# Optimization experiments

Hardware: AMD Instinct MI355X
Metric: run time of the kernel (lower is better)

Reference implementation:

```python
import jax, jax.numpy as jnp
import numpy as np

T = 0.2          # temperature
W = 0.1          # loss weight
BIG = 2 ** 30    # sentinel label for masked-out samples


def setup_inputs() -> dict:
    key = jax.random.key(0)
    k1, k2, k3, k4 = jax.random.split(key, 4)
    bs, C, Gn, S = 32, 128, 256, 16
    grouped_features = jax.random.normal(k1, (bs, C, Gn, S), dtype=jnp.float32)
    # instance labels in [-1, 8): -1 = background
    proposal_instance_mask = jax.random.randint(k2, (bs, Gn, S), -1, 8, dtype=jnp.int32)
    # seed indices with duplicates possible (range 40 over 16 samples)
    grouped_indices = jax.random.randint(k3, (bs, Gn, S), 0, 40, dtype=jnp.int32)
    context_compen = jax.random.normal(k4, (1, C), dtype=jnp.float32)
    return {
        "proposal_instance_mask": proposal_instance_mask,
        "grouped_features": grouped_features,
        "grouped_indices": grouped_indices,
        "context_compen": context_compen,
    }


def _group_loss(feat, idx, lab, ctx):
    # feat: [S, C], idx: [S], lab: [S], ctx: [C]
    # NOTE: sum_{a,b} f_a . g_b / (n_f * n_g) == mean(f) . mean(g), so the
    # original tiny-mm contrastive loss reduces to pairwise dots of per-instance means.
    S, C = feat.shape
    pos = jnp.arange(S)
    # unique count of seed indices -> truncate to first u samples (as in torch code)
    si = jnp.sort(idx)
    u = 1 + jnp.sum(si[1:] != si[:-1])
    valid = pos < u
    lab_m = jnp.where(valid, lab, BIG)
    # per-group unique labels (sorted), jit-friendly
    sl = jnp.sort(lab_m)
    new = jnp.concatenate([jnp.ones((1,), bool), sl[1:] != sl[:-1]])
    cid = jnp.cumsum(new) - 1                      # compact id of each sorted label
    uniq = jnp.full((S,), BIG, sl.dtype).at[cid].set(sl)
    n_labels = jnp.sum(new & (sl != BIG))          # number of distinct valid labels
    has_bg = uniq[0] == -1                         # -1 sorts first if present
    # per-instance mean features via segment scatter-add
    comp = jnp.searchsorted(uniq, lab_m)           # sample -> compact instance slot
    sums = jnp.zeros((S, C), feat.dtype).at[comp].add(jnp.where(valid[:, None], feat, 0.0))
    cnts = jnp.zeros((S,), feat.dtype).at[comp].add(valid.astype(feat.dtype))
    means = sums / jnp.maximum(cnts, 1.0)[:, None]
    hb = has_bg.astype(jnp.int32)
    fg_count = n_labels - hb
    inst_num = fg_count + 1                        # bg slot always present
    # row 0 = bg mean (or context_compen if no bg), rows 1.. = fg means
    gidx = jnp.clip(pos + hb - 1, 0, S - 1)
    M = means[gidx]
    M = M.at[0].set(jnp.where(has_bg, M[0], ctx))
    inst_valid = pos < inst_num
    sim = (M @ M.T) / T                            # [S, S] tiny matmul of means
    sim_m = jnp.where(inst_valid[None, :], sim, -jnp.inf)
    lse = jax.scipy.special.logsumexp(sim_m, axis=1)
    li = lse - jnp.diagonal(sim)                   # -log(pos/(pos+neg)) per fg row
    fg_mask = inst_valid & (pos >= 1)
    gl = jnp.sum(jnp.where(fg_mask, li, 0.0)) / jnp.maximum(inst_num - 1, 1).astype(feat.dtype)
    return gl, fg_count >= 1


def reference(proposal_instance_mask, grouped_features, grouped_indices, context_compen):
    bs, C, Gn, S = grouped_features.shape
    feats = grouped_features.transpose(0, 2, 3, 1).reshape(-1, S, C)  # [G, S, C]
    idxs = grouped_indices.reshape(-1, S)
    labs = proposal_instance_mask.reshape(-1, S)
    ctx = context_compen[0]
    gl, gv = jax.vmap(lambda f, i, l: _group_loss(f, i, l, ctx))(feats, idxs, labs)
    gvf = gv.astype(gl.dtype)
    return jnp.sum(gl * gvf) / jnp.sum(gvf) * W
```

## Files before the change

kernel.cpp:

```cpp
#include <hip/hip_runtime.h>

#define GQ 8192

#define WPB 4
#define MROW 132
#define WSLICE (9 * MROW + 81 + 11)

__global__ __launch_bounds__(64 * WPB, 2) void group_loss_kernel(
    const int*   __restrict__ labs,
    const float* __restrict__ feats,
    const int*   __restrict__ idxs,
    const float* __restrict__ ctx,
    float2* __restrict__ ws)
{
    __shared__ float SH[WPB * WSLICE];

    const int l = threadIdx.x & 63;
    const int w = threadIdx.x >> 6;
    float* MM   = SH + w * WSLICE;
    float* SIMM = MM + 9 * MROW;

    const int flat = blockIdx.x * WPB + w;
    const int g  = ((flat & 7) << 10) | (flat >> 3);
    const int b  = g >> 8;
    const int gn = g & 255;
    const long fbase = (long)b * (128 * 256 * 16) + (long)gn * 16;

    const float* gp0 = feats + fbase + (long)l * 4096;
    const float* gp1 = gp0 + 64 * 4096;
    float4 A[4], B[4];
    #pragma unroll
    for (int q = 0; q < 4; ++q) A[q] = *(const float4*)(gp0 + q * 4);
    #pragma unroll
    for (int q = 0; q < 4; ++q) B[q] = *(const float4*)(gp1 + q * 4);
    const float cx0 = ctx[l], cx1 = ctx[l + 64];

    int lab_u[16], idx_u[16];
    #pragma unroll
    for (int s = 0; s < 16; ++s) {
        lab_u[s] = labs[g * 16 + s];
        idx_u[s] = idxs[g * 16 + s];
    }
    int u = 1;
    #pragma unroll
    for (int s = 1; s < 16; ++s) {
        bool dup = false;
        #pragma unroll
        for (int j = 0; j < s; ++j) dup = dup || (idx_u[j] == idx_u[s]);
        u += dup ? 0 : 1;
    }
    unsigned memb[9]; int cnt[9];
    #pragma unroll
    for (int r = 0; r < 9; ++r) {
        unsigned m = 0; int c = 0;
        #pragma unroll
        for (int s = 0; s < 16; ++s) {
            if (s < u && lab_u[s] == r - 1) { m |= (1u << s); ++c; }
        }
        memb[r] = m; cnt[r] = c;
    }
    const bool has_bg = cnt[0] > 0;
    int fg_count = 0, pm = 0;
    #pragma unroll
    for (int r = 1; r < 9; ++r) {
        if (cnt[r] > 0) { ++fg_count; pm |= 1 << r; }
    }

    float m0[9], m1[9];
    #pragma unroll
    for (int r = 0; r < 9; ++r) {
        float a = 0.0f, bb = 0.0f;
        const unsigned m = memb[r];
        #pragma unroll
        for (int q = 0; q < 4; ++q) {
            if (m & (1u << (4 * q + 0))) { a += A[q].x; bb += B[q].x; }
            if (m & (1u << (4 * q + 1))) { a += A[q].y; bb += B[q].y; }
            if (m & (1u << (4 * q + 2))) { a += A[q].z; bb += B[q].z; }
            if (m & (1u << (4 * q + 3))) { a += A[q].w; bb += B[q].w; }
        }
        const float invc = 1.0f / (float)(cnt[r] > 0 ? cnt[r] : 1);
        m0[r] = a * invc;
        m1[r] = bb * invc;
    }
    if (!has_bg) { m0[0] = cx0; m1[0] = cx1; }

    #pragma unroll
    for (int r = 0; r < 9; ++r) {
        MM[r * MROW + l]      = m0[r];
        MM[r * MROW + 64 + l] = m1[r];
    }
    __syncthreads();

    float simv = 0.0f; int pi = 0, pj = 0;
    if (l < 44) {
        pi = (int)((sqrtf(8.0f * (float)l + 9.0f) - 1.0f) * 0.5f);
        pj = l - (pi * (pi + 1) / 2 - 1);
        const float* Ri = MM + pi * MROW;
        const float* Rj = MM + pj * MROW;
        float acc = 0.0f;
        #pragma unroll
        for (int q = 0; q < 32; ++q) {
            float4 x = *(const float4*)(Ri + 4 * q);
            float4 y = *(const float4*)(Rj + 4 * q);
            acc += x.x * y.x + x.y * y.y + x.z * y.z + x.w * y.w;
        }
        simv = acc * 5.0f;
    }
    if (l < 44) {
        SIMM[pi * 9 + pj] = simv;
        if (pi != pj) SIMM[pj * 9 + pi] = simv;
    }
    __syncthreads();

    float li_val = 0.0f;
    if (l >= 1 && l < 9 && ((pm >> l) & 1)) {
        float srow[9];
        #pragma unroll
        for (int j = 0; j < 9; ++j) srow[j] = SIMM[l * 9 + j];
        float vmax = srow[0];
        #pragma unroll
        for (int j = 1; j < 9; ++j)
            if ((pm >> j) & 1) vmax = fmaxf(vmax, srow[j]);
        float se = __expf(srow[0] - vmax);
        #pragma unroll
        for (int j = 1; j < 9; ++j)
            if ((pm >> j) & 1) se += __expf(srow[j] - vmax);
        li_val = vmax + __logf(se) - srow[l];
    }

    float ssum = li_val;
    #pragma unroll
    for (int off = 8; off >= 1; off >>= 1) ssum += __shfl_down(ssum, off);
    if (l == 0) {
        float2 r;
        r.x = ssum / (float)(fg_count > 0 ? fg_count : 1);
        r.y = (fg_count > 0) ? 1.0f : 0.0f;
        ws[g] = r;
    }
}

__global__ __launch_bounds__(1024) void reduce_kernel(
    const float2* __restrict__ ws, float* __restrict__ out)
{
    __shared__ float sa[1024], sb[1024];
    const int t = threadIdx.x;
    float a = 0.0f, b2 = 0.0f;
    for (int g = t; g < GQ; g += 1024) {
        float2 v = ws[g];
        a += v.x; b2 += v.y;
    }
    sa[t] = a; sb[t] = b2;
    __syncthreads();
    for (int off = 512; off > 0; off >>= 1) {
        if (t < off) { sa[t] += sa[t + off]; sb[t] += sb[t + off]; }
        __syncthreads();
    }
    if (t == 0) out[0] = 0.1f * (sa[0] / sb[0]);
}

extern "C" void kernel_launch(void* const* d_in, const int* in_sizes, int n_in,
                              void* d_out, int out_size, void* d_ws, size_t ws_size,
                              hipStream_t stream) {
    const int*   labs  = (const int*)d_in[0];
    const float* feats = (const float*)d_in[1];
    const int*   idxs  = (const int*)d_in[2];
    const float* ctx   = (const float*)d_in[3];
    float* out = (float*)d_out;
    float2* ws = (float2*)d_ws;

    group_loss_kernel<<<GQ / WPB, 64 * WPB, 0, stream>>>(labs, feats, idxs, ctx, ws);
    reduce_kernel<<<1, 1024, 0, stream>>>(ws, out);
}
```

Baseline: 128.6 us.

## Restructure feature loads for coalescing and transpose through LDS

```diff
diff --git a/kernel.cpp b/kernel.cpp
--- a/kernel.cpp
+++ b/kernel.cpp
@@ -1,39 +1,35 @@
 #include <hip/hip_runtime.h>
 
-#define GQ 8192
+#define GQ   8192
+#define WPB  4
+#define FROW 132
+#define SLICE 2144
 
-#define WPB 4
-#define MROW 132
-#define WSLICE (9 * MROW + 81 + 11)
-
-__global__ __launch_bounds__(64 * WPB, 2) void group_loss_kernel(
+__global__ __launch_bounds__(64 * WPB, 4) void group_loss_kernel(
     const int*   __restrict__ labs,
     const float* __restrict__ feats,
     const int*   __restrict__ idxs,
     const float* __restrict__ ctx,
     float2* __restrict__ ws)
 {
-    __shared__ float SH[WPB * WSLICE];
+    __shared__ float SH[WPB * SLICE];
 
-    const int l = threadIdx.x & 63;
-    const int w = threadIdx.x >> 6;
-    float* MM   = SH + w * WSLICE;
-    float* SIMM = MM + 9 * MROW;
+    const int l  = threadIdx.x & 63;
+    const int wu = __builtin_amdgcn_readfirstlane(threadIdx.x >> 6);
+    float* F    = SH + wu * SLICE;
+    float* MM   = F;
+    float* SIMM = F + 9 * FROW;
 
-    const int flat = blockIdx.x * WPB + w;
-    const int g  = ((flat & 7) << 10) | (flat >> 3);
+    const int blk = blockIdx.x;
+    const int g  = ((blk & 7) << 10) | ((blk >> 3) << 2) | wu;
     const int b  = g >> 8;
     const int gn = g & 255;
     const long fbase = (long)b * (128 * 256 * 16) + (long)gn * 16;
 
-    const float* gp0 = feats + fbase + (long)l * 4096;
-    const float* gp1 = gp0 + 64 * 4096;
-    float4 A[4], B[4];
+    const float* gp = feats + fbase + (long)((l >> 2) * 4096 + (l & 3) * 4);
+    float4 v[8];
     #pragma unroll
-    for (int q = 0; q < 4; ++q) A[q] = *(const float4*)(gp0 + q * 4);
-    #pragma unroll
-    for (int q = 0; q < 4; ++q) B[q] = *(const float4*)(gp1 + q * 4);
-    const float cx0 = ctx[l], cx1 = ctx[l + 64];
+    for (int i = 0; i < 8; ++i) v[i] = *(const float4*)(gp + (long)i * 65536);
 
     int lab_u[16], idx_u[16];
     #pragma unroll
@@ -66,17 +62,36 @@
         if (cnt[r] > 0) { ++fg_count; pm |= 1 << r; }
     }
 
+    {
+        const int c = 16 * 0 + (l >> 2);
+        const int s0 = 4 * (l & 3);
+        #pragma unroll
+        for (int i = 0; i < 8; ++i) {
+            const int cc = c + 16 * i;
+            F[(s0 + 0) * FROW + cc] = v[i].x;
+            F[(s0 + 1) * FROW + cc] = v[i].y;
+            F[(s0 + 2) * FROW + cc] = v[i].z;
+            F[(s0 + 3) * FROW + cc] = v[i].w;
+        }
+    }
+    __syncthreads();
+
+    float fa[16], fb[16];
+    #pragma unroll
+    for (int s = 0; s < 16; ++s) {
+        fa[s] = F[s * FROW + l];
+        fb[s] = F[s * FROW + 64 + l];
+    }
+    const float cx0 = ctx[l], cx1 = ctx[l + 64];
+
     float m0[9], m1[9];
     #pragma unroll
     for (int r = 0; r < 9; ++r) {
         float a = 0.0f, bb = 0.0f;
         const unsigned m = memb[r];
         #pragma unroll
-        for (int q = 0; q < 4; ++q) {
-            if (m & (1u << (4 * q + 0))) { a += A[q].x; bb += B[q].x; }
-            if (m & (1u << (4 * q + 1))) { a += A[q].y; bb += B[q].y; }
-            if (m & (1u << (4 * q + 2))) { a += A[q].z; bb += B[q].z; }
-            if (m & (1u << (4 * q + 3))) { a += A[q].w; bb += B[q].w; }
+        for (int s = 0; s < 16; ++s) {
+            if (m & (1u << s)) { a += fa[s]; bb += fb[s]; }
         }
         const float invc = 1.0f / (float)(cnt[r] > 0 ? cnt[r] : 1);
         m0[r] = a * invc;
@@ -84,10 +99,12 @@
     }
     if (!has_bg) { m0[0] = cx0; m1[0] = cx1; }
 
+    __syncthreads();
+
     #pragma unroll
     for (int r = 0; r < 9; ++r) {
-        MM[r * MROW + l]      = m0[r];
-        MM[r * MROW + 64 + l] = m1[r];
+        MM[r * FROW + l]      = m0[r];
+        MM[r * FROW + 64 + l] = m1[r];
     }
     __syncthreads();
 
@@ -95,8 +112,8 @@
     if (l < 44) {
         pi = (int)((sqrtf(8.0f * (float)l + 9.0f) - 1.0f) * 0.5f);
         pj = l - (pi * (pi + 1) / 2 - 1);
-        const float* Ri = MM + pi * MROW;
-        const float* Rj = MM + pj * MROW;
+        const float* Ri = MM + pi * FROW;
+        const float* Rj = MM + pj * FROW;
         float acc = 0.0f;
         #pragma unroll
         for (int q = 0; q < 32; ++q) {
```

After: 123.7 us. -3.8%, faster.

## Use wave ballots for dedup/membership and shrink blocks to two waves

Applied to the files above, without the earlier changes.

```diff
diff --git a/kernel.cpp b/kernel.cpp
--- a/kernel.cpp
+++ b/kernel.cpp
@@ -1,27 +1,26 @@
 #include <hip/hip_runtime.h>
 
-#define GQ 8192
+#define GQ   8192
+#define WPB  2
+#define MROW 132
+#define SLICE 1280
 
-#define WPB 4
-#define MROW 132
-#define WSLICE (9 * MROW + 81 + 11)
-
-__global__ __launch_bounds__(64 * WPB, 2) void group_loss_kernel(
+__global__ __launch_bounds__(64 * WPB, 6) void group_loss_kernel(
     const int*   __restrict__ labs,
     const float* __restrict__ feats,
     const int*   __restrict__ idxs,
     const float* __restrict__ ctx,
     float2* __restrict__ ws)
 {
-    __shared__ float SH[WPB * WSLICE];
+    __shared__ float SH[WPB * SLICE];
 
-    const int l = threadIdx.x & 63;
-    const int w = threadIdx.x >> 6;
-    float* MM   = SH + w * WSLICE;
+    const int l  = threadIdx.x & 63;
+    const int wu = threadIdx.x >> 6;
+    float* MM   = SH + wu * SLICE;
     float* SIMM = MM + 9 * MROW;
 
-    const int flat = blockIdx.x * WPB + w;
-    const int g  = ((flat & 7) << 10) | (flat >> 3);
+    const int blk = blockIdx.x;
+    const int g  = ((blk & 7) << 10) | ((blk >> 3) << 1) | wu;
     const int b  = g >> 8;
     const int gn = g & 255;
     const long fbase = (long)b * (128 * 256 * 16) + (long)gn * 16;
@@ -34,53 +33,62 @@
     #pragma unroll
     for (int q = 0; q < 4; ++q) B[q] = *(const float4*)(gp1 + q * 4);
     const float cx0 = ctx[l], cx1 = ctx[l + 64];
+    float fa[16], fb[16];
+    #pragma unroll
+    for (int q = 0; q < 4; ++q) {
+        fa[4*q+0] = A[q].x; fa[4*q+1] = A[q].y; fa[4*q+2] = A[q].z; fa[4*q+3] = A[q].w;
+        fb[4*q+0] = B[q].x; fb[4*q+1] = B[q].y; fb[4*q+2] = B[q].z; fb[4*q+3] = B[q].w;
+    }
 
-    int lab_u[16], idx_u[16];
+    int myidx = -1, mylab = -2;
+    if (l < 16) { myidx = idxs[g * 16 + l]; mylab = labs[g * 16 + l]; }
+
+    bool dup = false;
     #pragma unroll
-    for (int s = 0; s < 16; ++s) {
-        lab_u[s] = labs[g * 16 + s];
-        idx_u[s] = idxs[g * 16 + s];
+    for (int j = 0; j < 15; ++j) {
+        const int vj = __shfl(myidx, j);
+        dup = dup || ((l > j) && (myidx == vj));
     }
-    int u = 1;
-    #pragma unroll
-    for (int s = 1; s < 16; ++s) {
-        bool dup = false;
-        #pragma unroll
-        for (int j = 0; j < s; ++j) dup = dup || (idx_u[j] == idx_u[s]);
-        u += dup ? 0 : 1;
-    }
-    unsigned memb[9]; int cnt[9];
+    const int u = __popcll(__ballot((l < 16) && !dup));
+
+    const bool valid = l < u;
+    const int bid = valid ? (mylab + 1) : 255;
+
+    unsigned long long memb[9]; int cnt[9];
     #pragma unroll
     for (int r = 0; r < 9; ++r) {
-        unsigned m = 0; int c = 0;
-        #pragma unroll
-        for (int s = 0; s < 16; ++s) {
-            if (s < u && lab_u[s] == r - 1) { m |= (1u << s); ++c; }
-        }
-        memb[r] = m; cnt[r] = c;
+        memb[r] = __ballot(bid == r);
+        cnt[r]  = __popcll(memb[r]);
     }
     const bool has_bg = cnt[0] > 0;
     int fg_count = 0, pm = 0;
     #pragma unroll
-    for (int r = 1; r < 9; ++r) {
+    for (int r = 1; r < 9; ++r)
         if (cnt[r] > 0) { ++fg_count; pm |= 1 << r; }
+
+    float m0[9] = {0,0,0,0,0,0,0,0,0};
+    float m1[9] = {0,0,0,0,0,0,0,0,0};
+    #pragma unroll
+    for (int s = 0; s < 16; ++s) {
+        if (s < u) {
+            const int bs = __builtin_amdgcn_readlane(bid, s);
+            switch (bs) {
+                case 0: m0[0] += fa[s]; m1[0] += fb[s]; break;
+                case 1: m0[1] += fa[s]; m1[1] += fb[s]; break;
+                case 2: m0[2] += fa[s]; m1[2] += fb[s]; break;
+                case 3: m0[3] += fa[s]; m1[3] += fb[s]; break;
+                case 4: m0[4] += fa[s]; m1[4] += fb[s]; break;
+                case 5: m0[5] += fa[s]; m1[5] += fb[s]; break;
+                case 6: m0[6] += fa[s]; m1[6] += fb[s]; break;
+                case 7: m0[7] += fa[s]; m1[7] += fb[s]; break;
+                case 8: m0[8] += fa[s]; m1[8] += fb[s]; break;
+            }
+        }
     }
-
-    float m0[9], m1[9];
     #pragma unroll
     for (int r = 0; r < 9; ++r) {
-        float a = 0.0f, bb = 0.0f;
-        const unsigned m = memb[r];
-        #pragma unroll
-        for (int q = 0; q < 4; ++q) {
-            if (m & (1u << (4 * q + 0))) { a += A[q].x; bb += B[q].x; }
-            if (m & (1u << (4 * q + 1))) { a += A[q].y; bb += B[q].y; }
-            if (m & (1u << (4 * q + 2))) { a += A[q].z; bb += B[q].z; }
-            if (m & (1u << (4 * q + 3))) { a += A[q].w; bb += B[q].w; }
-        }
         const float invc = 1.0f / (float)(cnt[r] > 0 ? cnt[r] : 1);
-        m0[r] = a * invc;
-        m1[r] = bb * invc;
+        m0[r] *= invc; m1[r] *= invc;
     }
     if (!has_bg) { m0[0] = cx0; m1[0] = cx1; }
 
```

Result: faster. 112.0 us (-12.9%).
